# Kernel optimization log

Measured on AMD Instinct MI355X. Metric: run time of the kernel, lower is better.

The kernel has to match this reference:

```python
import jax, jax.numpy as jnp
import numpy as np

B, S, E, A = 32, 1000, 1024, 512


def setup_inputs() -> dict:
    key = jax.random.key(0)
    ks = jax.random.split(key, 7)
    sc = 0.02
    return {
        "x": jax.random.normal(ks[0], (B, S, E), dtype=jnp.float32),
        "Wk": jax.random.normal(ks[1], (E, A), dtype=jnp.float32) * sc,
        "bk": jax.random.normal(ks[2], (A,), dtype=jnp.float32) * sc,
        "Wq": jax.random.normal(ks[3], (E, A), dtype=jnp.float32) * sc,
        "bq": jax.random.normal(ks[4], (A,), dtype=jnp.float32) * sc,
        "Wv": jax.random.normal(ks[5], (E, A), dtype=jnp.float32) * sc,
        "bv": jax.random.normal(ks[6], (A,), dtype=jnp.float32) * sc,
    }


def reference(x, Wk, bk, Wq, bq, Wv, bv):
    seq = x.shape[1]
    k = x @ Wk + bk          # [B,S,A]
    q = x @ Wq + bq          # [B,S,A]
    v = x @ Wv + bv          # [B,S,A]
    # NOTE: module scales by sqrt(sequence), not sqrt(attention_dim)
    den = jnp.asarray(seq, x.dtype) ** 0.5
    scores = jnp.einsum("bqa,bka->bqk", q, k) / den  # [B,S,S]
    causal = jnp.tril(jnp.ones((seq, seq), dtype=bool))
    scores = jnp.where(causal, scores, -jnp.inf)
    attn = jax.nn.softmax(scores, axis=-1)
    return jnp.einsum("bqk,bka->bqa", attn, v)      # [B,S,A]
```

## Files before the change

### kernel.cpp

```cpp
#include <hip/hip_runtime.h>
#include <hip/hip_bf16.h>
#include <stdint.h>

#define DEVI __device__ __forceinline__

typedef short s16x8 __attribute__((ext_vector_type(8)));
typedef short s16x4 __attribute__((ext_vector_type(4)));
typedef float f32x4 __attribute__((ext_vector_type(4)));

static constexpr int BB = 32, SS = 1000, EE = 1024, AA = 512;
static constexpr int MM = BB * SS;

static constexpr size_t OFF_X16 = 0;
static constexpr size_t OFF_Q   = OFF_X16 + (size_t)MM * EE * 2;
static constexpr size_t OFF_K   = OFF_Q  + (size_t)MM * AA * 2;
static constexpr size_t OFF_VT  = OFF_K  + (size_t)MM * AA * 2;
static constexpr size_t OFF_WT  = OFF_VT + (size_t)BB * AA * SS * 2;

DEVI unsigned short f2bf(float f) {
  union { float f; unsigned int u; } c; c.f = f;
  unsigned int u = c.u + 0x7fffu + ((c.u >> 16) & 1u);
  return (unsigned short)(u >> 16);
}

DEVI void gl_lds16(const void* g, void* l) {
  __builtin_amdgcn_global_load_lds(
      (const __attribute__((address_space(1))) unsigned int*)g,
      (__attribute__((address_space(3))) unsigned int*)l, 16, 0, 0);
}

DEVI void wg_barrier() {
  asm volatile("" ::: "memory");
  __builtin_amdgcn_s_barrier();
  asm volatile("" ::: "memory");
}

DEVI float fast_exp2(float x) {
#if __has_builtin(__builtin_amdgcn_exp2f)
  return __builtin_amdgcn_exp2f(x);
#else
  return __builtin_exp2f(x);
#endif
}

__global__ __launch_bounds__(256) void x_to_bf16_kernel(const float* __restrict__ x,
                                                        unsigned short* __restrict__ x16) {
  const long n4 = (long)MM * EE / 4;
  long i = (long)blockIdx.x * blockDim.x + threadIdx.x;
  const long stride = (long)gridDim.x * blockDim.x;
  for (; i < n4; i += stride) {
    const float4 v = ((const float4*)x)[i];
    ushort4 o;
    o.x = f2bf(v.x); o.y = f2bf(v.y); o.z = f2bf(v.z); o.w = f2bf(v.w);
    ((ushort4*)x16)[i] = o;
  }
}

__global__ __launch_bounds__(256) void wt_kernel(const float* __restrict__ Wq,
                                                 const float* __restrict__ Wk,
                                                 const float* __restrict__ Wv,
                                                 unsigned short* __restrict__ WT) {
  const float* W = (blockIdx.z == 0) ? Wq : (blockIdx.z == 1) ? Wk : Wv;
  unsigned short* out = WT + (size_t)blockIdx.z * AA * EE;
  __shared__ unsigned short t[64][65];
  const int k0 = blockIdx.x * 64, n0 = blockIdx.y * 64;
  #pragma unroll
  for (int i = 0; i < 16; ++i) {
    int idx = i * 256 + threadIdx.x;
    int r = idx >> 6, c = idx & 63;
    t[r][c] = f2bf(W[(size_t)(k0 + r) * AA + n0 + c]);
  }
  __syncthreads();
  #pragma unroll
  for (int i = 0; i < 16; ++i) {
    int idx = i * 256 + threadIdx.x;
    int r = idx >> 6, c = idx & 63;
    out[(size_t)(n0 + r) * EE + k0 + c] = t[c][r];
  }
}

__global__ __launch_bounds__(256, 2) void proj_kernel(
    const unsigned short* __restrict__ X16, const unsigned short* __restrict__ WT,
    const float* __restrict__ bq, const float* __restrict__ bk, const float* __restrict__ bv,
    unsigned short* __restrict__ Qo, unsigned short* __restrict__ Ko,
    unsigned short* __restrict__ VTo) {
  constexpr int BK = 64, NKT = EE / BK;
  __shared__ unsigned char lds[65536];
  unsigned char* ldsA = lds;
  unsigned char* ldsB = lds + 32768;
  const int tid = threadIdx.x, lane = tid & 63, wave = tid >> 6;
  const int id = blockIdx.x;
  const int r12 = id % 12;
  const int z = r12 >> 2;
  const int m0 = (id / 12) * 128, n0 = (r12 & 3) * 128;
  const unsigned short* Wz = WT + (size_t)z * AA * EE;

  f32x4 acc[4][4];
  #pragma unroll
  for (int i = 0; i < 4; ++i)
    #pragma unroll
    for (int j = 0; j < 4; ++j) acc[i][j] = f32x4{0.f, 0.f, 0.f, 0.f};

  auto stage = [&](int buf, int kt) {
    #pragma unroll
    for (int i = 0; i < 4; ++i) {
      int c = i * 256 + tid;
      int row = c >> 3;
      int cb = ((c & 7) * 16) ^ ((row & 7) << 4);
      gl_lds16(X16 + (size_t)(m0 + row) * EE + kt * BK + (cb >> 1), ldsA + buf * 16384 + c * 16);
    }
    #pragma unroll
    for (int i = 0; i < 4; ++i) {
      int c = i * 256 + tid;
      int row = c >> 3;
      int cb = ((c & 7) * 16) ^ ((row & 7) << 4);
      gl_lds16(Wz + (size_t)(n0 + row) * EE + kt * BK + (cb >> 1), ldsB + buf * 16384 + c * 16);
    }
  };

  auto compute = [&](int buf) {
    #pragma unroll
    for (int kk = 0; kk < 2; ++kk) {
      s16x8 a[4], b[4];
      #pragma unroll
      for (int m = 0; m < 4; ++m) {
        int row = (wave >> 1) * 64 + m * 16 + (lane & 15);
        int cb = (kk * 64 + (lane >> 4) * 16) ^ ((row & 7) << 4);
        a[m] = *(const s16x8*)(ldsA + buf * 16384 + row * 128 + cb);
      }
      #pragma unroll
      for (int n = 0; n < 4; ++n) {
        int row = (wave & 1) * 64 + n * 16 + (lane & 15);
        int cb = (kk * 64 + (lane >> 4) * 16) ^ ((row & 7) << 4);
        b[n] = *(const s16x8*)(ldsB + buf * 16384 + row * 128 + cb);
      }
      #pragma unroll
      for (int m = 0; m < 4; ++m)
        #pragma unroll
        for (int n = 0; n < 4; ++n)
          acc[m][n] = __builtin_amdgcn_mfma_f32_16x16x32_bf16(a[m], b[n], acc[m][n], 0, 0, 0);
    }
  };

  stage(0, 0);
  for (int kt = 0; kt < NKT; ++kt) {
    const int cur = kt & 1;
    if (kt + 1 < NKT) {
      stage(cur ^ 1, kt + 1);
      asm volatile("s_waitcnt vmcnt(8)" ::: "memory");
    } else {
      asm volatile("s_waitcnt vmcnt(0)" ::: "memory");
    }
    wg_barrier();
    compute(cur);
    wg_barrier();
  }

  const float* bias = (z == 0) ? bq : (z == 1) ? bk : bv;
  const float scale = (z == 0) ? 0.04562280215f : 1.0f;
  unsigned short* T = (unsigned short*)lds;
  const int rbase = (wave >> 1) * 64 + (lane >> 4) * 4;
  const int cbase = (wave & 1) * 64 + (lane & 15);
  float bvals[4];
  #pragma unroll
  for (int n = 0; n < 4; ++n) bvals[n] = bias[n0 + cbase + n * 16];
  #pragma unroll
  for (int m = 0; m < 4; ++m) {
    #pragma unroll
    for (int n = 0; n < 4; ++n) {
      const int cl = cbase + n * 16;
      #pragma unroll
      for (int j = 0; j < 4; ++j) {
        const int rl = rbase + m * 16 + j;
        const unsigned short h = f2bf((acc[m][n][j] + bvals[n]) * scale);
        if (z == 2) T[cl * 136 + rl] = h;
        else        T[rl * 136 + cl] = h;
      }
    }
  }
  wg_barrier();
  #pragma unroll
  for (int i = 0; i < 8; ++i) {
    int c2 = i * 256 + tid;
    int r = c2 >> 4, ch = (c2 & 15) * 8;
    s16x8 chunk = *(const s16x8*)&T[r * 136 + ch];
    if (z == 2) {
      const int rowg0 = m0 + ch;
      const int bb2 = rowg0 / SS, ss2 = rowg0 - bb2 * SS;
      *(s16x8*)&VTo[(size_t)bb2 * AA * SS + (size_t)(n0 + r) * SS + ss2] = chunk;
    } else {
      unsigned short* O = (z == 0) ? Qo : Ko;
      *(s16x8*)&O[(size_t)(m0 + r) * AA + n0 + ch] = chunk;
    }
  }
}

__global__ __launch_bounds__(512, 2) void attn_kernel(
    const unsigned short* __restrict__ Qs, const unsigned short* __restrict__ Ks,
    const unsigned short* __restrict__ VT, float* __restrict__ out) {
  constexpr int KVB = 32;
  __shared__ unsigned char ldsK[2][KVB * AA * 2];
  __shared__ unsigned char ldsV[2][AA * KVB * 2];
  __shared__ unsigned char ldsP[8][16 * 80];

  const int tid = threadIdx.x, lane = tid & 63, wave = tid >> 6;
  const int L = blockIdx.x;
  const int b = L & 31;
  const int g = 7 - (L >> 5);
  const int q0w = g * 128 + wave * 16;

  const unsigned short* kbase = Ks + (size_t)b * SS * AA;
  const unsigned short* vbase = VT + (size_t)b * AA * SS;
  unsigned int koff[4], voff[4];
  #pragma unroll
  for (int i = 0; i < 4; ++i) {
    int c = i * 512 + tid;
    int r = c >> 6;
    int cb = ((c & 63) * 16) ^ ((r & 7) << 4);
    koff[i] = r * AA + (cb >> 1);
    int pair = c >> 3;
    int within = (c & 7) * 16;
    int half = within >> 6;
    int kb = (within & 63) ^ ((pair & 3) << 4);
    int a_ = pair * 2 + half;
    voff[i] = a_ * SS + (kb >> 1);
  }

  s16x8 qf[16];
  {
    int qrow = q0w + (lane & 15);
    int qr = qrow < SS ? qrow : SS - 1;
    const unsigned short* qp = Qs + (size_t)(b * SS + qr) * AA + (lane >> 4) * 8;
    #pragma unroll
    for (int f = 0; f < 16; ++f) qf[f] = *(const s16x8*)(qp + f * 32);
  }

  f32x4 o[32];
  #pragma unroll
  for (int n = 0; n < 32; ++n) o[n] = f32x4{0.f, 0.f, 0.f, 0.f};
  float mrun[4], ps[4];
  #pragma unroll
  for (int j = 0; j < 4; ++j) { mrun[j] = -__builtin_inff(); ps[j] = 0.f; }

  const int kmax = (g * 128 + 128 < SS) ? g * 128 + 128 : SS;
  const int ntiles = (kmax + KVB - 1) / KVB;

  auto stageKV = [&](int buf, int t) {
    #pragma unroll
    for (int i = 0; i < 4; ++i)
      gl_lds16(kbase + koff[i] + (unsigned)(t * (KVB * AA)),
               &ldsK[buf][(i * 512 + tid) * 16]);
    #pragma unroll
    for (int i = 0; i < 4; ++i)
      gl_lds16(vbase + voff[i] + (unsigned)(t * KVB),
               &ldsV[buf][(i * 512 + tid) * 16]);
  };

  stageKV(0, 0);
  asm volatile("s_waitcnt vmcnt(0)" ::: "memory");
  wg_barrier();

  for (int t = 0; t < ntiles; ++t) {
    const int cur = t & 1;
    const int k0 = t * KVB;
    if (t + 1 < ntiles) stageKV(cur ^ 1, t + 1);

    f32x4 p0a = {0.f, 0.f, 0.f, 0.f}, p0b = {0.f, 0.f, 0.f, 0.f};
    f32x4 p1a = {0.f, 0.f, 0.f, 0.f}, p1b = {0.f, 0.f, 0.f, 0.f};
    {
      const int r0 = lane & 15;
      const int sw = (r0 & 7) << 4;
      const int kb16 = (lane >> 4) * 16;
      const int rb0 = r0 << 10, rb1 = (r0 + 16) << 10;
      #pragma unroll
      for (int f = 0; f < 8; ++f) {
        const int offA = f * 64 + kb16;
        const int offB = (f + 8) * 64 + kb16;
        s16x8 k0A = *(const s16x8*)&ldsK[cur][rb0 + (offA ^ sw)];
        s16x8 k1A = *(const s16x8*)&ldsK[cur][rb1 + (offA ^ sw)];
        s16x8 k0B = *(const s16x8*)&ldsK[cur][rb0 + (offB ^ sw)];
        s16x8 k1B = *(const s16x8*)&ldsK[cur][rb1 + (offB ^ sw)];
        p0a = __builtin_amdgcn_mfma_f32_16x16x32_bf16(qf[f], k0A, p0a, 0, 0, 0);
        p1a = __builtin_amdgcn_mfma_f32_16x16x32_bf16(qf[f], k1A, p1a, 0, 0, 0);
        p0b = __builtin_amdgcn_mfma_f32_16x16x32_bf16(qf[f + 8], k0B, p0b, 0, 0, 0);
        p1b = __builtin_amdgcn_mfma_f32_16x16x32_bf16(qf[f + 8], k1B, p1b, 0, 0, 0);
      }
    }
    f32x4 p0 = p0a + p0b, p1 = p1a + p1b;

    const int kcol = k0 + (lane & 15);
    float lm[4];
    #pragma unroll
    for (int j = 0; j < 4; ++j) {
      const int q = q0w + (lane >> 4) * 4 + j;
      float s0 = p0[j], s1 = p1[j];
      if (kcol > q || kcol >= SS) s0 = -__builtin_inff();
      if (kcol + 16 > q || kcol + 16 >= SS) s1 = -__builtin_inff();
      p0[j] = s0; p1[j] = s1;
      lm[j] = fmaxf(s0, s1);
    }
    const int myneed = (lm[0] > mrun[0] + 8.f) | (lm[1] > mrun[1] + 8.f) |
                       (lm[2] > mrun[2] + 8.f) | (lm[3] > mrun[3] + 8.f);
    if (__any(myneed)) {
      float rm[4] = {lm[0], lm[1], lm[2], lm[3]};
      #pragma unroll
      for (int st = 1; st <= 8; st <<= 1)
        #pragma unroll
        for (int j = 0; j < 4; ++j) rm[j] = fmaxf(rm[j], __shfl_xor(rm[j], st));
      float corr[4];
      #pragma unroll
      for (int j = 0; j < 4; ++j) {
        const float mnew = fmaxf(mrun[j], rm[j]);
        corr[j] = fast_exp2(mrun[j] - mnew);
        mrun[j] = mnew;
        ps[j] *= corr[j];
      }
      #pragma unroll
      for (int n = 0; n < 32; ++n)
        #pragma unroll
        for (int j = 0; j < 4; ++j) o[n][j] *= corr[j];
    }
    #pragma unroll
    for (int j = 0; j < 4; ++j) {
      const float e0 = fast_exp2(p0[j] - mrun[j]);
      const float e1 = fast_exp2(p1[j] - mrun[j]);
      ps[j] += e0 + e1;
      p0[j] = e0; p1[j] = e1;
    }

    {
      unsigned short* pb = (unsigned short*)&ldsP[wave][0];
      const int prow = (lane >> 4) * 4, pc = lane & 15;
      #pragma unroll
      for (int j = 0; j < 4; ++j) {
        pb[(prow + j) * 40 + pc]      = f2bf(p0[j]);
        pb[(prow + j) * 40 + pc + 16] = f2bf(p1[j]);
      }
    }
    s16x8 pa;
    {
      const unsigned char* pp = &ldsP[wave][(lane & 15) * 80 + (lane >> 4) * 16];
      s16x4 lo = *(const s16x4*)pp;
      s16x4 hi = *(const s16x4*)(pp + 8);
      pa = s16x8{lo[0], lo[1], lo[2], lo[3], hi[0], hi[1], hi[2], hi[3]};
    }

    #pragma unroll
    for (int n = 0; n < 32; ++n) {
      const int a_ = n * 16 + (lane & 15);
      const int pair = a_ >> 1;
      const int off = pair * 128 + (a_ & 1) * 64 + (((lane >> 4) * 16) ^ ((pair & 3) << 4));
      s16x8 vb = *(const s16x8*)&ldsV[cur][off];
      o[n] = __builtin_amdgcn_mfma_f32_16x16x32_bf16(pa, vb, o[n], 0, 0, 0);
    }

    asm volatile("s_waitcnt vmcnt(0)" ::: "memory");
    wg_barrier();
  }

  #pragma unroll
  for (int st = 1; st <= 8; st <<= 1)
    #pragma unroll
    for (int j = 0; j < 4; ++j) ps[j] += __shfl_xor(ps[j], st);
  #pragma unroll
  for (int j = 0; j < 4; ++j) {
    const int q = q0w + (lane >> 4) * 4 + j;
    if (q < SS) {
      const float inv = 1.0f / ps[j];
      float* op = out + (size_t)(b * SS + q) * AA + (lane & 15);
      #pragma unroll
      for (int n = 0; n < 32; ++n) op[n * 16] = o[n][j] * inv;
    }
  }
}

extern "C" void kernel_launch(void* const* d_in, const int* in_sizes, int n_in,
                              void* d_out, int out_size, void* d_ws, size_t ws_size,
                              hipStream_t stream) {
  const float* x  = (const float*)d_in[0];
  const float* Wk = (const float*)d_in[1];
  const float* bk = (const float*)d_in[2];
  const float* Wq = (const float*)d_in[3];
  const float* bq = (const float*)d_in[4];
  const float* Wv = (const float*)d_in[5];
  const float* bv = (const float*)d_in[6];

  char* ws = (char*)d_ws;
  unsigned short* X16 = (unsigned short*)(ws + OFF_X16);
  unsigned short* Qw  = (unsigned short*)(ws + OFF_Q);
  unsigned short* Kw  = (unsigned short*)(ws + OFF_K);
  unsigned short* VTw = (unsigned short*)(ws + OFF_VT);
  unsigned short* WT  = (unsigned short*)(ws + OFF_WT);

  x_to_bf16_kernel<<<dim3(2048), dim3(256), 0, stream>>>(x, X16);
  wt_kernel<<<dim3(EE / 64, AA / 64, 3), dim3(256), 0, stream>>>(Wq, Wk, Wv, WT);
  proj_kernel<<<dim3(3000), dim3(256), 0, stream>>>(
      X16, WT, bq, bk, bv, Qw, Kw, VTw);
  attn_kernel<<<dim3(256), dim3(512), 0, stream>>>(Qw, Kw, VTw, (float*)d_out);
}
```

Measured before the change: 318.0 us.

## Split long causal query blocks across workgroups and merge partials in combine kernel

Balances causal attention work by capping each workgroup's first phase at 20 KV tiles. Workgroups for short query blocks (g<=2) take a second phase that processes the remaining KV tiles of a long block (g>=5). The partial outputs plus running max and sum are written to the reused X16 workspace, and a new combine kernel merges the two partials with a log-sum-exp rescale. This is meant to cut the tail imbalance where the last query blocks dominate kernel time, at the cost of extra partial-buffer traffic and an extra kernel launch.

```diff
diff --git a/kernel.cpp b/kernel.cpp
--- a/kernel.cpp
+++ b/kernel.cpp
@@ -16,6 +16,9 @@
 static constexpr size_t OFF_K   = OFF_Q  + (size_t)MM * AA * 2;
 static constexpr size_t OFF_VT  = OFF_K  + (size_t)MM * AA * 2;
 static constexpr size_t OFF_WT  = OFF_VT + (size_t)BB * AA * SS * 2;
+
+static constexpr int PROWS = BB * 3 * 128;
+static constexpr size_t ML_OFF = (size_t)2 * PROWS * 512;
 
 DEVI unsigned short f2bf(float f) {
   union { float f; unsigned int u; } c; c.f = f;
@@ -197,7 +200,8 @@
 
 __global__ __launch_bounds__(512, 2) void attn_kernel(
     const unsigned short* __restrict__ Qs, const unsigned short* __restrict__ Ks,
-    const unsigned short* __restrict__ VT, float* __restrict__ out) {
+    const unsigned short* __restrict__ VT, float* __restrict__ out,
+    float* __restrict__ part) {
   constexpr int KVB = 32;
   __shared__ unsigned char ldsK[2][KVB * AA * 2];
   __shared__ unsigned char ldsV[2][AA * KVB * 2];
@@ -207,7 +211,6 @@
   const int L = blockIdx.x;
   const int b = L & 31;
   const int g = 7 - (L >> 5);
-  const int q0w = g * 128 + wave * 16;
 
   const unsigned short* kbase = Ks + (size_t)b * SS * AA;
   const unsigned short* vbase = VT + (size_t)b * AA * SS;
@@ -226,25 +229,6 @@
     voff[i] = a_ * SS + (kb >> 1);
   }
 
-  s16x8 qf[16];
-  {
-    int qrow = q0w + (lane & 15);
-    int qr = qrow < SS ? qrow : SS - 1;
-    const unsigned short* qp = Qs + (size_t)(b * SS + qr) * AA + (lane >> 4) * 8;
-    #pragma unroll
-    for (int f = 0; f < 16; ++f) qf[f] = *(const s16x8*)(qp + f * 32);
-  }
-
-  f32x4 o[32];
-  #pragma unroll
-  for (int n = 0; n < 32; ++n) o[n] = f32x4{0.f, 0.f, 0.f, 0.f};
-  float mrun[4], ps[4];
-  #pragma unroll
-  for (int j = 0; j < 4; ++j) { mrun[j] = -__builtin_inff(); ps[j] = 0.f; }
-
-  const int kmax = (g * 128 + 128 < SS) ? g * 128 + 128 : SS;
-  const int ntiles = (kmax + KVB - 1) / KVB;
-
   auto stageKV = [&](int buf, int t) {
     #pragma unroll
     for (int i = 0; i < 4; ++i)
@@ -256,122 +240,199 @@
                &ldsV[buf][(i * 512 + tid) * 16]);
   };
 
-  stageKV(0, 0);
-  asm volatile("s_waitcnt vmcnt(0)" ::: "memory");
-  wg_barrier();
-
-  for (int t = 0; t < ntiles; ++t) {
-    const int cur = t & 1;
-    const int k0 = t * KVB;
-    if (t + 1 < ntiles) stageKV(cur ^ 1, t + 1);
-
-    f32x4 p0a = {0.f, 0.f, 0.f, 0.f}, p0b = {0.f, 0.f, 0.f, 0.f};
-    f32x4 p1a = {0.f, 0.f, 0.f, 0.f}, p1b = {0.f, 0.f, 0.f, 0.f};
+  int ownN = 4 * (g + 1);
+  int rb_[2], t0_[2], t1_[2], md_[2], cx_[2];
+  int nph = 1;
+  rb_[0] = 128 * g; t0_[0] = 0; t1_[0] = (ownN < 20) ? ownN : 20;
+  md_[0] = (g <= 4) ? 0 : 1; cx_[0] = g - 5;
+  if (g <= 2) {
+    int r = 7 - g;
+    rb_[1] = 128 * r; t0_[1] = 20; t1_[1] = 4 * (r + 1); md_[1] = 2; cx_[1] = r - 5;
+    nph = 2;
+  }
+
+  for (int ph = 0; ph < nph; ++ph) {
+    const int rowbase = rb_[ph], tbeg = t0_[ph], tend = t1_[ph];
+    const int mode = md_[ph], cidx = cx_[ph];
+    const int q0w = rowbase + wave * 16;
+
+    s16x8 qf[16];
     {
-      const int r0 = lane & 15;
-      const int sw = (r0 & 7) << 4;
-      const int kb16 = (lane >> 4) * 16;
-      const int rb0 = r0 << 10, rb1 = (r0 + 16) << 10;
-      #pragma unroll
-      for (int f = 0; f < 8; ++f) {
-        const int offA = f * 64 + kb16;
-        const int offB = (f + 8) * 64 + kb16;
-        s16x8 k0A = *(const s16x8*)&ldsK[cur][rb0 + (offA ^ sw)];
-        s16x8 k1A = *(const s16x8*)&ldsK[cur][rb1 + (offA ^ sw)];
-        s16x8 k0B = *(const s16x8*)&ldsK[cur][rb0 + (offB ^ sw)];
-        s16x8 k1B = *(const s16x8*)&ldsK[cur][rb1 + (offB ^ sw)];
-        p0a = __builtin_amdgcn_mfma_f32_16x16x32_bf16(qf[f], k0A, p0a, 0, 0, 0);
-        p1a = __builtin_amdgcn_mfma_f32_16x16x32_bf16(qf[f], k1A, p1a, 0, 0, 0);
-        p0b = __builtin_amdgcn_mfma_f32_16x16x32_bf16(qf[f + 8], k0B, p0b, 0, 0, 0);
-        p1b = __builtin_amdgcn_mfma_f32_16x16x32_bf16(qf[f + 8], k1B, p1b, 0, 0, 0);
-      }
-    }
-    f32x4 p0 = p0a + p0b, p1 = p1a + p1b;
-
-    const int kcol = k0 + (lane & 15);
-    float lm[4];
-    #pragma unroll
-    for (int j = 0; j < 4; ++j) {
-      const int q = q0w + (lane >> 4) * 4 + j;
-      float s0 = p0[j], s1 = p1[j];
-      if (kcol > q || kcol >= SS) s0 = -__builtin_inff();
-      if (kcol + 16 > q || kcol + 16 >= SS) s1 = -__builtin_inff();
-      p0[j] = s0; p1[j] = s1;
-      lm[j] = fmaxf(s0, s1);
-    }
-    const int myneed = (lm[0] > mrun[0] + 8.f) | (lm[1] > mrun[1] + 8.f) |
-                       (lm[2] > mrun[2] + 8.f) | (lm[3] > mrun[3] + 8.f);
-    if (__any(myneed)) {
-      float rm[4] = {lm[0], lm[1], lm[2], lm[3]};
-      #pragma unroll
-      for (int st = 1; st <= 8; st <<= 1)
-        #pragma unroll
-        for (int j = 0; j < 4; ++j) rm[j] = fmaxf(rm[j], __shfl_xor(rm[j], st));
-      float corr[4];
-      #pragma unroll
-      for (int j = 0; j < 4; ++j) {
-        const float mnew = fmaxf(mrun[j], rm[j]);
-        corr[j] = fast_exp2(mrun[j] - mnew);
-        mrun[j] = mnew;
-        ps[j] *= corr[j];
-      }
-      #pragma unroll
-      for (int n = 0; n < 32; ++n)
-        #pragma unroll
-        for (int j = 0; j < 4; ++j) o[n][j] *= corr[j];
-    }
-    #pragma unroll
-    for (int j = 0; j < 4; ++j) {
-      const float e0 = fast_exp2(p0[j] - mrun[j]);
-      const float e1 = fast_exp2(p1[j] - mrun[j]);
-      ps[j] += e0 + e1;
-      p0[j] = e0; p1[j] = e1;
-    }
-
-    {
-      unsigned short* pb = (unsigned short*)&ldsP[wave][0];
-      const int prow = (lane >> 4) * 4, pc = lane & 15;
-      #pragma unroll
-      for (int j = 0; j < 4; ++j) {
-        pb[(prow + j) * 40 + pc]      = f2bf(p0[j]);
-        pb[(prow + j) * 40 + pc + 16] = f2bf(p1[j]);
-      }
-    }
-    s16x8 pa;
-    {
-      const unsigned char* pp = &ldsP[wave][(lane & 15) * 80 + (lane >> 4) * 16];
-      s16x4 lo = *(const s16x4*)pp;
-      s16x4 hi = *(const s16x4*)(pp + 8);
-      pa = s16x8{lo[0], lo[1], lo[2], lo[3], hi[0], hi[1], hi[2], hi[3]};
-    }
-
-    #pragma unroll
-    for (int n = 0; n < 32; ++n) {
-      const int a_ = n * 16 + (lane & 15);
-      const int pair = a_ >> 1;
-      const int off = pair * 128 + (a_ & 1) * 64 + (((lane >> 4) * 16) ^ ((pair & 3) << 4));
-      s16x8 vb = *(const s16x8*)&ldsV[cur][off];
-      o[n] = __builtin_amdgcn_mfma_f32_16x16x32_bf16(pa, vb, o[n], 0, 0, 0);
-    }
-
+      int qrow = q0w + (lane & 15);
+      int qr = qrow < SS ? qrow : SS - 1;
+      const unsigned short* qp = Qs + (size_t)(b * SS + qr) * AA + (lane >> 4) * 8;
+      #pragma unroll
+      for (int f = 0; f < 16; ++f) qf[f] = *(const s16x8*)(qp + f * 32);
+    }
+
+    f32x4 o[32];
+    #pragma unroll
+    for (int n = 0; n < 32; ++n) o[n] = f32x4{0.f, 0.f, 0.f, 0.f};
+    float mrun[4], ps[4];
+    #pragma unroll
+    for (int j = 0; j < 4; ++j) { mrun[j] = -__builtin_inff(); ps[j] = 0.f; }
+
+    stageKV(0, tbeg);
     asm volatile("s_waitcnt vmcnt(0)" ::: "memory");
     wg_barrier();
-  }
-
-  #pragma unroll
-  for (int st = 1; st <= 8; st <<= 1)
-    #pragma unroll
-    for (int j = 0; j < 4; ++j) ps[j] += __shfl_xor(ps[j], st);
-  #pragma unroll
-  for (int j = 0; j < 4; ++j) {
-    const int q = q0w + (lane >> 4) * 4 + j;
-    if (q < SS) {
-      const float inv = 1.0f / ps[j];
-      float* op = out + (size_t)(b * SS + q) * AA + (lane & 15);
-      #pragma unroll
-      for (int n = 0; n < 32; ++n) op[n * 16] = o[n][j] * inv;
-    }
-  }
+
+    for (int t = tbeg; t < tend; ++t) {
+      const int cur = (t - tbeg) & 1;
+      const int k0 = t * KVB;
+      if (t + 1 < tend) stageKV(cur ^ 1, t + 1);
+
+      f32x4 p0a = {0.f, 0.f, 0.f, 0.f}, p0b = {0.f, 0.f, 0.f, 0.f};
+      f32x4 p1a = {0.f, 0.f, 0.f, 0.f}, p1b = {0.f, 0.f, 0.f, 0.f};
+      {
+        const int r0 = lane & 15;
+        const int sw = (r0 & 7) << 4;
+        const int kb16 = (lane >> 4) * 16;
+        const int rb0 = r0 << 10, rb1 = (r0 + 16) << 10;
+        #pragma unroll
+        for (int f = 0; f < 8; ++f) {
+          const int offA = f * 64 + kb16;
+          const int offB = (f + 8) * 64 + kb16;
+          s16x8 k0A = *(const s16x8*)&ldsK[cur][rb0 + (offA ^ sw)];
+          s16x8 k1A = *(const s16x8*)&ldsK[cur][rb1 + (offA ^ sw)];
+          s16x8 k0B = *(const s16x8*)&ldsK[cur][rb0 + (offB ^ sw)];
+          s16x8 k1B = *(const s16x8*)&ldsK[cur][rb1 + (offB ^ sw)];
+          p0a = __builtin_amdgcn_mfma_f32_16x16x32_bf16(qf[f], k0A, p0a, 0, 0, 0);
+          p1a = __builtin_amdgcn_mfma_f32_16x16x32_bf16(qf[f], k1A, p1a, 0, 0, 0);
+          p0b = __builtin_amdgcn_mfma_f32_16x16x32_bf16(qf[f + 8], k0B, p0b, 0, 0, 0);
+          p1b = __builtin_amdgcn_mfma_f32_16x16x32_bf16(qf[f + 8], k1B, p1b, 0, 0, 0);
+        }
+      }
+      f32x4 p0 = p0a + p0b, p1 = p1a + p1b;
+
+      const int kcol = k0 + (lane & 15);
+      float lm[4];
+      #pragma unroll
+      for (int j = 0; j < 4; ++j) {
+        const int q = q0w + (lane >> 4) * 4 + j;
+        float s0 = p0[j], s1 = p1[j];
+        if (kcol > q || kcol >= SS) s0 = -__builtin_inff();
+        if (kcol + 16 > q || kcol + 16 >= SS) s1 = -__builtin_inff();
+        p0[j] = s0; p1[j] = s1;
+        lm[j] = fmaxf(s0, s1);
+      }
+      const int myneed = (lm[0] > mrun[0] + 8.f) | (lm[1] > mrun[1] + 8.f) |
+                         (lm[2] > mrun[2] + 8.f) | (lm[3] > mrun[3] + 8.f);
+      if (__any(myneed)) {
+        float rm[4] = {lm[0], lm[1], lm[2], lm[3]};
+        #pragma unroll
+        for (int st = 1; st <= 8; st <<= 1)
+          #pragma unroll
+          for (int j = 0; j < 4; ++j) rm[j] = fmaxf(rm[j], __shfl_xor(rm[j], st));
+        float corr[4];
+        #pragma unroll
+        for (int j = 0; j < 4; ++j) {
+          const float mnew = fmaxf(mrun[j], rm[j]);
+          corr[j] = fast_exp2(mrun[j] - mnew);
+          mrun[j] = mnew;
+          ps[j] *= corr[j];
+        }
+        #pragma unroll
+        for (int n = 0; n < 32; ++n)
+          #pragma unroll
+          for (int j = 0; j < 4; ++j) o[n][j] *= corr[j];
+      }
+      #pragma unroll
+      for (int j = 0; j < 4; ++j) {
+        const float e0 = fast_exp2(p0[j] - mrun[j]);
+        const float e1 = fast_exp2(p1[j] - mrun[j]);
+        ps[j] += e0 + e1;
+        p0[j] = e0; p1[j] = e1;
+      }
+
+      {
+        unsigned short* pb = (unsigned short*)&ldsP[wave][0];
+        const int prow = (lane >> 4) * 4, pc = lane & 15;
+        #pragma unroll
+        for (int j = 0; j < 4; ++j) {
+          pb[(prow + j) * 40 + pc]      = f2bf(p0[j]);
+          pb[(prow + j) * 40 + pc + 16] = f2bf(p1[j]);
+        }
+      }
+      s16x8 pa;
+      {
+        const unsigned char* pp = &ldsP[wave][(lane & 15) * 80 + (lane >> 4) * 16];
+        s16x4 lo = *(const s16x4*)pp;
+        s16x4 hi = *(const s16x4*)(pp + 8);
+        pa = s16x8{lo[0], lo[1], lo[2], lo[3], hi[0], hi[1], hi[2], hi[3]};
+      }
+
+      #pragma unroll
+      for (int n = 0; n < 32; ++n) {
+        const int a_ = n * 16 + (lane & 15);
+        const int pair = a_ >> 1;
+        const int off = pair * 128 + (a_ & 1) * 64 + (((lane >> 4) * 16) ^ ((pair & 3) << 4));
+        s16x8 vb = *(const s16x8*)&ldsV[cur][off];
+        o[n] = __builtin_amdgcn_mfma_f32_16x16x32_bf16(pa, vb, o[n], 0, 0, 0);
+      }
+
+      asm volatile("s_waitcnt vmcnt(0)" ::: "memory");
+      wg_barrier();
+    }
+
+    #pragma unroll
+    for (int st = 1; st <= 8; st <<= 1)
+      #pragma unroll
+      for (int j = 0; j < 4; ++j) ps[j] += __shfl_xor(ps[j], st);
+
+    if (mode == 0) {
+      #pragma unroll
+      for (int j = 0; j < 4; ++j) {
+        const int q = q0w + (lane >> 4) * 4 + j;
+        if (q < SS) {
+          const float inv = 1.0f / ps[j];
+          float* op = out + (size_t)(b * SS + q) * AA + (lane & 15);
+          #pragma unroll
+          for (int n = 0; n < 32; ++n) op[n * 16] = o[n][j] * inv;
+        }
+      }
+    } else {
+      const int slot = mode - 1;
+      #pragma unroll
+      for (int j = 0; j < 4; ++j) {
+        const int rl = wave * 16 + (lane >> 4) * 4 + j;
+        const size_t idx = (size_t)slot * PROWS + ((size_t)(b * 3 + cidx) * 128 + rl);
+        float* po = part + idx * 512 + (lane & 15);
+        #pragma unroll
+        for (int n = 0; n < 32; ++n) po[n * 16] = o[n][j];
+        if ((lane & 15) == 0) {
+          float* pml = part + ML_OFF + idx * 2;
+          pml[0] = mrun[j];
+          pml[1] = ps[j];
+        }
+      }
+    }
+  }
+}
+
+__global__ __launch_bounds__(256) void combine_kernel(const float* __restrict__ part,
+                                                      float* __restrict__ out) {
+  const int rid = blockIdx.x * 2 + (threadIdx.x >> 7);
+  const int t = threadIdx.x & 127;
+  const int b = rid / 384;
+  const int rem = rid - b * 384;
+  const int c = rem >> 7, row = rem & 127;
+  const int q = (c + 5) * 128 + row;
+  if (q >= SS) return;
+  const float* mlA = part + ML_OFF + (size_t)rid * 2;
+  const float* mlB = part + ML_OFF + ((size_t)PROWS + rid) * 2;
+  const float mA = mlA[0], lA = mlA[1];
+  const float mB = mlB[0], lB = mlB[1];
+  const float m = fmaxf(mA, mB);
+  const float sA = fast_exp2(mA - m), sB = fast_exp2(mB - m);
+  const float inv = 1.0f / (lA * sA + lB * sB);
+  const float4 a = ((const float4*)(part + (size_t)rid * 512))[t];
+  const float4 d = ((const float4*)(part + ((size_t)PROWS + rid) * 512))[t];
+  float4 r;
+  r.x = (a.x * sA + d.x * sB) * inv;
+  r.y = (a.y * sA + d.y * sB) * inv;
+  r.z = (a.z * sA + d.z * sB) * inv;
+  r.w = (a.w * sA + d.w * sB) * inv;
+  ((float4*)(out + ((size_t)b * SS + q) * AA))[t] = r;
 }
 
 extern "C" void kernel_launch(void* const* d_in, const int* in_sizes, int n_in,
@@ -391,10 +452,12 @@
   unsigned short* Kw  = (unsigned short*)(ws + OFF_K);
   unsigned short* VTw = (unsigned short*)(ws + OFF_VT);
   unsigned short* WT  = (unsigned short*)(ws + OFF_WT);
+  float* Part = (float*)(ws + OFF_X16);
 
   x_to_bf16_kernel<<<dim3(2048), dim3(256), 0, stream>>>(x, X16);
   wt_kernel<<<dim3(EE / 64, AA / 64, 3), dim3(256), 0, stream>>>(Wq, Wk, Wv, WT);
   proj_kernel<<<dim3(3000), dim3(256), 0, stream>>>(
       X16, WT, bq, bk, bv, Qw, Kw, VTw);
-  attn_kernel<<<dim3(256), dim3(512), 0, stream>>>(Qw, Kw, VTw, (float*)d_out);
-}
+  attn_kernel<<<dim3(256), dim3(512), 0, stream>>>(Qw, Kw, VTw, (float*)d_out, Part);
+  combine_kernel<<<dim3(PROWS / 2), dim3(256), 0, stream>>>(Part, (float*)d_out);
+}
```

Result: faster. 301.1 us (-5.3%).
